# Kernel tuning notes

Hardware: AMD Instinct MI355X
Metric: run time of the kernel (lower is better)

The kernel has to match this reference:

```python
import jax, jax.numpy as jnp
import numpy as np

B, T, E, H, A, V = 32, 128, 256, 512, 256, 32000
S_SRC, S_CUE = 64, 64
OUT_IN = E + 2 * H + 2 * H  # emb + rnn_out + knowledge + src_ctx + cue_ctx (memory_size=H)
NEG = -1e9


def setup_inputs() -> dict:
    key = jax.random.key(0)
    ks = jax.random.split(key, 20)
    s = lambda k, sh: (jax.random.normal(k, sh) / np.sqrt(sh[0])).astype(jnp.float32)
    inp = {}
    inp['tokens'] = jax.random.randint(ks[0], (B, T), 0, V)
    inp['lengths'] = jax.random.randint(ks[1], (B,), 1, T + 1)
    inp['hidden0'] = jax.random.normal(ks[2], (B, H)) * 0.1
    inp['knowledge'] = jax.random.normal(ks[3], (B, H)) * 0.1
    inp['src_mem'] = jax.random.normal(ks[4], (B, S_SRC, H)) * 0.1
    inp['src_lengths'] = jax.random.randint(ks[5], (B,), 1, S_SRC + 1)
    inp['cue_mem'] = jax.random.normal(ks[6], (B, S_CUE, H)) * 0.1
    inp['cue_lengths'] = jax.random.randint(ks[7], (B,), 1, S_CUE + 1)
    # parameters
    inp['emb'] = jax.random.normal(ks[8], (V, E)) * 0.02
    inp['w_ih'] = s(ks[9], (E, 3 * H)); inp['w_hh'] = s(ks[10], (H, 3 * H))
    inp['b_ih'] = jnp.zeros((3 * H,)); inp['b_hh'] = jnp.zeros((3 * H,))
    Q = E + 2 * H
    inp['src_wq'] = s(ks[11], (Q, A)); inp['src_bq'] = jnp.zeros((A,))
    inp['src_wm'] = s(ks[12], (H, A)); inp['src_v'] = s(ks[13], (A,))
    inp['cue_wq'] = s(ks[14], (Q, A)); inp['cue_bq'] = jnp.zeros((A,))
    inp['cue_wm'] = s(ks[15], (H, A)); inp['cue_v'] = s(ks[16], (A,))
    inp['w_out1'] = s(ks[17], (OUT_IN, H)); inp['b_out1'] = jnp.zeros((H,))
    inp['w_out2'] = s(ks[18], (H, V)); inp['b_out2'] = jnp.zeros((V,))
    return inp


def _mlp_attn(q, mk, mem, wq, bq, v, mask):
    # q: (B,Q), mk = mem@wm precomputed: (B,S,A), mem: (B,S,H), mask: (B,S) True=valid
    scores = jnp.einsum('bsa,a->bs', jnp.tanh((q @ wq + bq)[:, None, :] + mk), v)
    scores = jnp.where(mask, scores, NEG)
    w = jax.nn.softmax(scores, axis=-1)
    return jnp.einsum('bs,bsh->bh', w, mem)


def reference(tokens, lengths, hidden0, knowledge, src_mem, src_lengths, cue_mem,
              cue_lengths, emb, w_ih, w_hh, b_ih, b_hh, src_wq, src_bq, src_wm,
              src_v, cue_wq, cue_bq, cue_wm, cue_v, w_out1, b_out1, w_out2, b_out2):
    x_all = emb[tokens]                                   # (B,T,E) teacher-forced embeddings
    valid = jnp.arange(T)[None, :] < lengths[:, None]     # (B,T)
    src_mask = jnp.arange(S_SRC)[None, :] < src_lengths[:, None]
    cue_mask = jnp.arange(S_CUE)[None, :] < cue_lengths[:, None]
    src_mk = src_mem @ src_wm                             # (B,S,A) hoisted memory projection
    cue_mk = cue_mem @ cue_wm

    def step(h, xs):
        x, vm = xs                                        # (B,E), (B,)
        gi = x @ w_ih + b_ih
        gh = h @ w_hh + b_hh
        i_r, i_z, i_n = jnp.split(gi, 3, axis=-1)
        h_r, h_z, h_n = jnp.split(gh, 3, axis=-1)
        r = jax.nn.sigmoid(i_r + h_r)
        z = jax.nn.sigmoid(i_z + h_z)
        n = jnp.tanh(i_n + r * h_n)
        h_new = (1.0 - z) * n + z * h                     # torch GRU cell
        q = jnp.concatenate([x, h, knowledge], axis=-1)   # query uses OLD hidden (as in source)
        src_ctx = _mlp_attn(q, src_mk, src_mem, src_wq, src_bq, src_v, src_mask)
        cue_ctx = _mlp_attn(q, cue_mk, cue_mem, cue_wq, cue_bq, cue_v, cue_mask)
        out_in = jnp.concatenate([x, h_new, knowledge, src_ctx, cue_ctx], axis=-1)
        vmc = vm[:, None]
        h_next = jnp.where(vmc, h_new, h)                 # only valid rows advance (length-sorted loop)
        return h_next, (jnp.where(vmc, out_in, 0.0), jnp.where(vmc, h_new, 0.0))

    h_final, (out_inputs, hid_mem) = jax.lax.scan(
        step, hidden0, (x_all.transpose(1, 0, 2), valid.T))
    out_inputs = out_inputs.transpose(1, 0, 2)            # (B,T,OUT_IN)
    hidden_memory = hid_mem.transpose(1, 0, 2)            # (B,T,H)
    logits = (out_inputs @ w_out1 + b_out1) @ w_out2 + b_out2
    log_probs = jax.nn.log_softmax(logits, axis=-1)       # (B,T,V)
    return log_probs, hidden_memory, h_final
```

## Files before the change

### kernel.cpp

```cpp
#include <hip/hip_runtime.h>

typedef unsigned int uint;
typedef unsigned short ushort;
using short8 = __attribute__((ext_vector_type(8))) short;
using f32x4  = __attribute__((ext_vector_type(4))) float;

#define DEVFN __device__ __forceinline__

constexpr int B_ = 32, T_ = 128, E_ = 256, H_ = 512, A_ = 256, V_ = 32000, S_ = 64;
constexpr int G3_ = 3 * H_;
constexpr int OUTIN_ = E_ + 4 * H_;
constexpr int M_ = B_ * T_;

DEVFN ushort f2b(float f) {
  uint u = __float_as_uint(f);
  u += 0x7fffu + ((u >> 16) & 1u);
  return (ushort)(u >> 16);
}
DEVFN float b2f(ushort b) { return __uint_as_float(((uint)b) << 16); }
DEVFN float sigmoid_f(float x) { return 1.f / (1.f + __expf(-x)); }
DEVFN float tanh_f(float x) { float e = __expf(2.f * x); return 1.f - 2.f / (e + 1.f); }

__global__ __launch_bounds__(256) void transpose_k(const float* __restrict__ in,
                                                   ushort* __restrict__ out, int R, int C) {
  __shared__ __align__(16) ushort tile[64][65];
  int c0 = blockIdx.x * 64, r0 = blockIdx.y * 64;
  int tx = threadIdx.x & 63, ty = threadIdx.x >> 6;
#pragma unroll
  for (int k = 0; k < 16; k++) {
    int i = ty + k * 4;
    int r = r0 + i, c = c0 + tx;
    if (r < R && c < C) tile[tx][i] = f2b(in[(size_t)r * C + c]);
  }
  __syncthreads();
#pragma unroll
  for (int k = 0; k < 16; k++) {
    int j = ty + k * 4;
    int c = c0 + j, r = r0 + tx;
    if (r < R && c < C) out[(size_t)c * R + r] = tile[j][tx];
  }
}

__global__ void convert_k(const float* __restrict__ in, ushort* __restrict__ out, int n) {
  int i = blockIdx.x * 256 + threadIdx.x;
  if (i < n) out[i] = f2b(in[i]);
}

__global__ __launch_bounds__(256) void gather_k(const int* __restrict__ tokens,
                                                const float* __restrict__ emb,
                                                ushort* __restrict__ xbf) {
  int r = blockIdx.x;
  int t = r >> 5, b = r & 31;
  int tok = tokens[b * T_ + t];
  xbf[(size_t)r * E_ + threadIdx.x] = f2b(emb[(size_t)tok * E_ + threadIdx.x]);
}

__global__ __launch_bounds__(256) void kq_k(const float* __restrict__ knowledge,
                                            const float* __restrict__ wq,
                                            const float* __restrict__ bq,
                                            float* __restrict__ kq) {
  int b = blockIdx.x, a = threadIdx.x;
  const float* kn = knowledge + b * H_;
  float s = 0.f;
  for (int h = 0; h < H_; h++) s += kn[h] * wq[(size_t)(E_ + H_ + h) * A_ + a];
  kq[b * A_ + a] = s + bq[a];
}

template <int OUTBF, int PERM, int HASBIAS>
__global__ __launch_bounds__(256) void gemm_bt(const ushort* __restrict__ Ag,
                                               const ushort* __restrict__ Btg,
                                               const float* __restrict__ bias,
                                               void* __restrict__ Cg, int M, int N, int K) {
  __shared__ __align__(16) ushort Ash[128][40];
  __shared__ __align__(16) ushort Bsh[128][40];
  const int nbx = gridDim.x;
  const int nwg = nbx * gridDim.y;
  const int lin = blockIdx.y * nbx + blockIdx.x;
  const int cpx = nwg >> 3;
  const int swz = (lin & 7) * cpx + (lin >> 3);
  const int m0 = (swz / nbx) * 128, n0 = (swz % nbx) * 128;
  const int tid = threadIdx.x;
  const int wave = tid >> 6, lane = tid & 63, lr = lane & 15, lg = lane >> 4;
  const int wr = wave >> 1, wc = wave & 1;
  f32x4 acc[4][4] = {};
  for (int kk = 0; kk < K; kk += 32) {
    {
      int r = tid >> 2, q = tid & 3;
      *(short8*)&Ash[r][q * 8] = *(const short8*)&Ag[(size_t)(m0 + r) * K + kk + q * 8];
      *(short8*)&Bsh[r][q * 8] = *(const short8*)&Btg[(size_t)(n0 + r) * K + kk + q * 8];
      r += 64;
      *(short8*)&Ash[r][q * 8] = *(const short8*)&Ag[(size_t)(m0 + r) * K + kk + q * 8];
      *(short8*)&Bsh[r][q * 8] = *(const short8*)&Btg[(size_t)(n0 + r) * K + kk + q * 8];
    }
    __syncthreads();
    short8 af[4], bfr[4];
#pragma unroll
    for (int mi = 0; mi < 4; mi++) af[mi] = *(const short8*)&Ash[wr * 64 + mi * 16 + lr][lg * 8];
#pragma unroll
    for (int ni = 0; ni < 4; ni++) bfr[ni] = *(const short8*)&Bsh[wc * 64 + ni * 16 + lr][lg * 8];
#pragma unroll
    for (int mi = 0; mi < 4; mi++)
#pragma unroll
      for (int ni = 0; ni < 4; ni++)
        acc[mi][ni] = __builtin_amdgcn_mfma_f32_16x16x32_bf16(af[mi], bfr[ni], acc[mi][ni], 0, 0, 0);
    __syncthreads();
  }
#pragma unroll
  for (int mi = 0; mi < 4; mi++)
#pragma unroll
    for (int ni = 0; ni < 4; ni++) {
      int col = n0 + wc * 64 + ni * 16 + lr;
      float bv = HASBIAS ? bias[col] : 0.f;
#pragma unroll
      for (int r = 0; r < 4; r++) {
        int row = m0 + wr * 64 + mi * 16 + lg * 4 + r;
        int orow = PERM ? ((row & 31) << 7) + (row >> 5) : row;
        float v = acc[mi][ni][r] + bv;
        if (OUTBF == 1)      ((ushort*)Cg)[(size_t)orow * N + col] = f2b(v);
        else if (OUTBF == 2) ((ushort*)Cg)[(size_t)orow * 2 * N + col] = f2b(v);
        else                 ((float*)Cg)[(size_t)orow * N + col] = v;
      }
    }
}

__global__ void inith_k(const float* __restrict__ h0, ushort* __restrict__ hpb) {
  int g = blockIdx.x * 256 + threadIdx.x;
  hpb[g] = f2b(h0[g]);
}

__global__ __launch_bounds__(128, 1) void scan_k(
    const float* __restrict__ w_hh, const float* __restrict__ b_hh,
    const float* __restrict__ gi, const int* __restrict__ lengths,
    const float* __restrict__ h0, ushort* hpb,
    float* __restrict__ hidmem, float* __restrict__ hfinal, uint* flags) {
  __shared__ __align__(16) ushort pk[2][16][16];
  const int wg = blockIdx.x;
  const int c0 = wg * 16;
  const int tid = threadIdx.x;
  const int wave = tid >> 6, lane = tid & 63, lr = lane & 15, lg = lane >> 4;
  const int c = c0 + lr;

  short8 wf0[16], wf1[16], wf2[16];
#pragma unroll
  for (int kk = 0; kk < 16; kk++) {
    short8 v0, v1, v2;
#pragma unroll
    for (int i = 0; i < 8; i++) {
      int k = kk * 32 + lg * 8 + i;
      v0[i] = (short)f2b(w_hh[(size_t)k * G3_ + 0 * H_ + c]);
      v1[i] = (short)f2b(w_hh[(size_t)k * G3_ + 1 * H_ + c]);
      v2[i] = (short)f2b(w_hh[(size_t)k * G3_ + 2 * H_ + c]);
    }
    wf0[kk] = v0; wf1[kk] = v1; wf2[kk] = v2;
  }
  const float bh0 = b_hh[c], bh1 = b_hh[H_ + c], bh2 = b_hh[2 * H_ + c];
  int len[4];
  float hp[4];
#pragma unroll
  for (int r = 0; r < 4; r++) {
    int bt = 16 * wave + lg * 4 + r;
    len[r] = lengths[bt];
    hp[r] = h0[(size_t)bt * H_ + c];
  }

  const uint fidx = ((uint)(lane & 31) * 2 + (uint)wave) * 32;

#pragma unroll 1
  for (int t = 0; t < T_; t++) {
    float g0[4], g1[4], g2[4];
#pragma unroll
    for (int r = 0; r < 4; r++) {
      int bt = 16 * wave + lg * 4 + r;
      const float* gr = gi + (size_t)(t * 32 + bt) * G3_ + c;
      g0[r] = gr[0]; g1[r] = gr[H_]; g2[r] = gr[2 * H_];
    }
    if (t > 0) {
      while (true) {
        uint f = __hip_atomic_load(&flags[fidx], __ATOMIC_RELAXED, __HIP_MEMORY_SCOPE_AGENT);
        if (__all((int)(f >= (uint)t))) break;
        __builtin_amdgcn_s_sleep(1);
      }
    }
    asm volatile("" ::: "memory");

    const ushort* Sb = hpb + (size_t)t * (B_ * H_);
    const int rowA = 16 * wave + lr;
    f32x4 a0 = {}, a1 = {}, a2 = {};
#pragma unroll
    for (int kk = 0; kk < 16; kk++) {
      short8 av = *(const short8*)(Sb + rowA * H_ + kk * 32 + lg * 8);
      a0 = __builtin_amdgcn_mfma_f32_16x16x32_bf16(av, wf0[kk], a0, 0, 0, 0);
      a1 = __builtin_amdgcn_mfma_f32_16x16x32_bf16(av, wf1[kk], a1, 0, 0, 0);
      a2 = __builtin_amdgcn_mfma_f32_16x16x32_bf16(av, wf2[kk], a2, 0, 0, 0);
    }

    ushort* Un16 = hpb + (size_t)(t + 1) * (B_ * H_);
    float hmv[4];
#pragma unroll
    for (int r = 0; r < 4; r++) {
      float rr = sigmoid_f(g0[r] + a0[r] + bh0);
      float zz = sigmoid_f(g1[r] + a1[r] + bh1);
      float nn = tanh_f(g2[r] + rr * (a2[r] + bh2));
      float hv = (1.f - zz) * nn + zz * hp[r];
      bool valid = t < len[r];
      float hx = valid ? hv : hp[r];
      hp[r] = hx;
      hmv[r] = valid ? hv : 0.f;
      pk[wave][lg * 4 + r][lr] = f2b(hx);
    }
    if (lane < 32) {
      int row = lane >> 1, half = lane & 1;
      short8 v = *(const short8*)&pk[wave][row][half * 8];
      ushort* gp = Un16 + ((size_t)(16 * wave + row) * H_ + c0 + half * 8);
      asm volatile("global_store_dwordx4 %0, %1, off sc1" :: "v"(gp), "v"(v) : "memory");
    }
    asm volatile("s_waitcnt vmcnt(0)" ::: "memory");
    if (lane == 0)
      __hip_atomic_store(&flags[(wg * 2 + wave) * 32], (uint)(t + 1),
                         __ATOMIC_RELAXED, __HIP_MEMORY_SCOPE_AGENT);
#pragma unroll
    for (int r = 0; r < 4; r++) {
      int bt = 16 * wave + lg * 4 + r;
      hidmem[((size_t)bt * T_ + t) * H_ + c] = hmv[r];
    }
  }
#pragma unroll
  for (int r = 0; r < 4; r++) {
    int bt = 16 * wave + lg * 4 + r;
    hfinal[(size_t)bt * H_ + c] = hp[r];
  }
}

__global__ __launch_bounds__(256) void attn_k(
    const float* __restrict__ qxk, const float* __restrict__ qh, const float* __restrict__ kq,
    const float* __restrict__ mk, const float* __restrict__ mem, const float* __restrict__ vvec,
    const int* __restrict__ slen, float* __restrict__ ctx) {
  __shared__ float qf[A_], vv[A_], sc[S_];
  int bx = blockIdx.x;
  int b = bx >> 7, t = bx & 127;
  int row = t * B_ + b;
  int tid = threadIdx.x;
  qf[tid] = qxk[(size_t)row * A_ + tid] + qh[(size_t)row * A_ + tid] + kq[b * A_ + tid];
  vv[tid] = vvec[tid];
  __syncthreads();
  int s = tid >> 2, q4 = tid & 3;
  const float* mkr = mk + ((size_t)(b * S_) + s) * A_;
  float part = 0.f;
#pragma unroll 4
  for (int i = 0; i < 64; i++) {
    int a = q4 + (i << 2);
    part += tanh_f(qf[a] + mkr[a]) * vv[a];
  }
  part += __shfl_xor(part, 1, 64);
  part += __shfl_xor(part, 2, 64);
  if (q4 == 0) sc[s] = part;
  __syncthreads();
  if (tid < S_) {
    float v = (tid < slen[b]) ? sc[tid] : -1e9f;
    float mm = v;
    for (int off = 1; off < 64; off <<= 1) mm = fmaxf(mm, __shfl_xor(mm, off, 64));
    float e = __expf(v - mm);
    float ss = e;
    for (int off = 1; off < 64; off <<= 1) ss += __shfl_xor(ss, off, 64);
    sc[tid] = e / ss;
  }
  __syncthreads();
  float c0 = 0.f, c1 = 0.f;
  const float* mb = mem + (size_t)b * S_ * H_;
  for (int ss2 = 0; ss2 < S_; ss2++) {
    float w = sc[ss2];
    c0 += w * mb[ss2 * H_ + tid];
    c1 += w * mb[ss2 * H_ + tid + 256];
  }
  ctx[(size_t)row * H_ + tid] = c0;
  ctx[(size_t)row * H_ + tid + 256] = c1;
}

__global__ __launch_bounds__(256) void assemble_k(
    const ushort* __restrict__ xbf, const float* __restrict__ hm,
    const float* __restrict__ knowledge, const float* __restrict__ ctxs,
    const float* __restrict__ ctxc, const int* __restrict__ lengths,
    ushort* __restrict__ outin) {
  int r = blockIdx.x;
  int t = r >> 5, b = r & 31;
  bool valid = t < lengths[b];
  int tid = threadIdx.x;
  ushort* dst = outin + (size_t)r * OUTIN_;
#pragma unroll
  for (int kblk = 0; kblk < 9; kblk++) {
    int i = kblk * 256 + tid;
    ushort v;
    if (i < E_)               v = xbf[(size_t)r * E_ + i];
    else if (i < E_ + H_)     v = f2b(hm[((size_t)b * T_ + t) * H_ + i - E_]);
    else if (i < E_ + 2 * H_) v = f2b(knowledge[b * H_ + i - (E_ + H_)]);
    else if (i < E_ + 3 * H_) v = f2b(ctxs[(size_t)r * H_ + i - (E_ + 2 * H_)]);
    else                      v = f2b(ctxc[(size_t)r * H_ + i - (E_ + 3 * H_)]);
    dst[i] = valid ? v : (ushort)0;
  }
}

__global__ __launch_bounds__(256) void logsoftmax_k(float* __restrict__ logits) {
  __shared__ float redm[4], reds[4];
  float* row = logits + (size_t)blockIdx.x * V_;
  const short8* rg = (const short8*)row;
  const int tid = threadIdx.x;
  short8 buf[16];
  float m = -3.4e38f, s = 0.f;
#pragma unroll
  for (int k = 0; k < 16; k++) {
    int i = tid + k * 256;
    if (i < V_ / 8) {
      short8 v = rg[i];
      buf[k] = v;
      float f0 = b2f((ushort)v[0]), f1 = b2f((ushort)v[1]);
      float f2 = b2f((ushort)v[2]), f3 = b2f((ushort)v[3]);
      float f4 = b2f((ushort)v[4]), f5 = b2f((ushort)v[5]);
      float f6 = b2f((ushort)v[6]), f7 = b2f((ushort)v[7]);
      float vm = fmaxf(fmaxf(fmaxf(f0, f1), fmaxf(f2, f3)),
                       fmaxf(fmaxf(f4, f5), fmaxf(f6, f7)));
      float nm = fmaxf(m, vm);
      s = s * __expf(m - nm) + __expf(f0 - nm) + __expf(f1 - nm) + __expf(f2 - nm) +
          __expf(f3 - nm) + __expf(f4 - nm) + __expf(f5 - nm) + __expf(f6 - nm) +
          __expf(f7 - nm);
      m = nm;
    }
  }
  for (int off = 1; off < 64; off <<= 1) {
    float om = __shfl_xor(m, off, 64), os = __shfl_xor(s, off, 64);
    float nm = fmaxf(m, om);
    s = s * __expf(m - nm) + os * __expf(om - nm);
    m = nm;
  }
  if ((tid & 63) == 0) { redm[tid >> 6] = m; reds[tid >> 6] = s; }
  __syncthreads();
  float M = fmaxf(fmaxf(redm[0], redm[1]), fmaxf(redm[2], redm[3]));
  float S = reds[0] * __expf(redm[0] - M) + reds[1] * __expf(redm[1] - M) +
            reds[2] * __expf(redm[2] - M) + reds[3] * __expf(redm[3] - M);
  float lse = M + __logf(S);
  __syncthreads();
#pragma unroll
  for (int k = 0; k < 16; k++) {
    int i = tid + k * 256;
    if (i < V_ / 8) {
      short8 v = buf[k];
      float4 o0, o1;
      o0.x = b2f((ushort)v[0]) - lse; o0.y = b2f((ushort)v[1]) - lse;
      o0.z = b2f((ushort)v[2]) - lse; o0.w = b2f((ushort)v[3]) - lse;
      o1.x = b2f((ushort)v[4]) - lse; o1.y = b2f((ushort)v[5]) - lse;
      o1.z = b2f((ushort)v[6]) - lse; o1.w = b2f((ushort)v[7]) - lse;
      *(float4*)&row[i * 8] = o0;
      *(float4*)&row[i * 8 + 4] = o1;
    }
  }
}

extern "C" void kernel_launch(void* const* d_in, const int* in_sizes, int n_in,
                              void* d_out, int out_size, void* d_ws, size_t ws_size,
                              hipStream_t stream) {
  const int*   tokens    = (const int*)  d_in[0];
  const int*   lengths   = (const int*)  d_in[1];
  const float* hidden0   = (const float*)d_in[2];
  const float* knowledge = (const float*)d_in[3];
  const float* src_mem   = (const float*)d_in[4];
  const int*   src_len   = (const int*)  d_in[5];
  const float* cue_mem   = (const float*)d_in[6];
  const int*   cue_len   = (const int*)  d_in[7];
  const float* emb       = (const float*)d_in[8];
  const float* w_ih      = (const float*)d_in[9];
  const float* w_hh      = (const float*)d_in[10];
  const float* b_ih      = (const float*)d_in[11];
  const float* b_hh      = (const float*)d_in[12];
  const float* src_wq    = (const float*)d_in[13];
  const float* src_bq    = (const float*)d_in[14];
  const float* src_wm    = (const float*)d_in[15];
  const float* src_v     = (const float*)d_in[16];
  const float* cue_wq    = (const float*)d_in[17];
  const float* cue_bq    = (const float*)d_in[18];
  const float* cue_wm    = (const float*)d_in[19];
  const float* cue_v     = (const float*)d_in[20];
  const float* w_out1    = (const float*)d_in[21];
  const float* b_out1    = (const float*)d_in[22];
  const float* w_out2    = (const float*)d_in[23];
  const float* b_out2    = (const float*)d_in[24];

  float* out_lp = (float*)d_out;
  float* out_hm = out_lp + (size_t)M_ * V_;
  float* out_hf = out_hm + (size_t)M_ * H_;

  char* scb = (char*)d_out;
  size_t off = 0;
  auto alloc = [&](size_t bytes) -> void* {
    void* p = scb + off;
    off = (off + bytes + 255) & ~(size_t)255;
    return p;
  };
  float*  GI    = (float*) alloc((size_t)M_ * G3_ * 4);
  float*  QXKs  = (float*) alloc((size_t)M_ * A_ * 4);
  float*  QXKc  = (float*) alloc((size_t)M_ * A_ * 4);
  float*  QHs   = (float*) alloc((size_t)M_ * A_ * 4);
  float*  QHc   = (float*) alloc((size_t)M_ * A_ * 4);
  float*  CTXs  = (float*) alloc((size_t)M_ * H_ * 4);
  float*  CTXc  = (float*) alloc((size_t)M_ * H_ * 4);
  ushort* OUTIN = (ushort*)alloc((size_t)M_ * OUTIN_ * 2);
  ushort* XBF   = (ushort*)alloc((size_t)M_ * E_ * 2);
  ushort* WIHT  = (ushort*)alloc((size_t)G3_ * E_ * 2);
  ushort* WQXTs = (ushort*)alloc((size_t)A_ * E_ * 2);
  ushort* WQXTc = (ushort*)alloc((size_t)A_ * E_ * 2);
  ushort* WQHTs = (ushort*)alloc((size_t)A_ * H_ * 2);
  ushort* WQHTc = (ushort*)alloc((size_t)A_ * H_ * 2);
  ushort* WMTs  = (ushort*)alloc((size_t)A_ * H_ * 2);
  ushort* WMTc  = (ushort*)alloc((size_t)A_ * H_ * 2);
  ushort* WO1T  = (ushort*)alloc((size_t)H_ * OUTIN_ * 2);
  ushort* MEMBs = (ushort*)alloc((size_t)B_ * S_ * H_ * 2);
  ushort* MEMBc = (ushort*)alloc((size_t)B_ * S_ * H_ * 2);
  float*  MKs   = (float*) alloc((size_t)B_ * S_ * A_ * 4);
  float*  MKc   = (float*) alloc((size_t)B_ * S_ * A_ * 4);
  float*  KQs   = (float*) alloc((size_t)B_ * A_ * 4);
  float*  KQc   = (float*) alloc((size_t)B_ * A_ * 4);
  ushort* HPB   = (ushort*)alloc((size_t)(T_ + 1) * B_ * H_ * 2);

  uint* FLAGS = (uint*)d_ws;
  ushort* WO2T = (ushort*)((char*)d_ws + 8192);
  ushort* HID1 = (ushort*)((char*)d_ws + 8192 + (size_t)V_ * H_ * 2);

  dim3 blk(256);
  hipMemsetAsync(FLAGS, 0, 8192, stream);

  transpose_k<<<dim3(G3_ / 64, E_ / 64), blk, 0, stream>>>(w_ih, WIHT, E_, G3_);
  transpose_k<<<dim3(A_ / 64, E_ / 64), blk, 0, stream>>>(src_wq, WQXTs, E_, A_);
  transpose_k<<<dim3(A_ / 64, H_ / 64), blk, 0, stream>>>(src_wq + (size_t)E_ * A_, WQHTs, H_, A_);
  transpose_k<<<dim3(A_ / 64, E_ / 64), blk, 0, stream>>>(cue_wq, WQXTc, E_, A_);
  transpose_k<<<dim3(A_ / 64, H_ / 64), blk, 0, stream>>>(cue_wq + (size_t)E_ * A_, WQHTc, H_, A_);
  transpose_k<<<dim3(A_ / 64, H_ / 64), blk, 0, stream>>>(src_wm, WMTs, H_, A_);
  transpose_k<<<dim3(A_ / 64, H_ / 64), blk, 0, stream>>>(cue_wm, WMTc, H_, A_);
  transpose_k<<<dim3(H_ / 64, OUTIN_ / 64), blk, 0, stream>>>(w_out1, WO1T, OUTIN_, H_);
  transpose_k<<<dim3(V_ / 64, H_ / 64), blk, 0, stream>>>(w_out2, WO2T, H_, V_);
  convert_k<<<(B_ * S_ * H_ + 255) / 256, blk, 0, stream>>>(src_mem, MEMBs, B_ * S_ * H_);
  convert_k<<<(B_ * S_ * H_ + 255) / 256, blk, 0, stream>>>(cue_mem, MEMBc, B_ * S_ * H_);

  gather_k<<<M_, blk, 0, stream>>>(tokens, emb, XBF);
  kq_k<<<B_, blk, 0, stream>>>(knowledge, src_wq, src_bq, KQs);
  kq_k<<<B_, blk, 0, stream>>>(knowledge, cue_wq, cue_bq, KQc);

  gemm_bt<0, 0, 1><<<dim3(G3_ / 128, M_ / 128), blk, 0, stream>>>(XBF, WIHT, b_ih, GI, M_, G3_, E_);
  gemm_bt<0, 0, 0><<<dim3(A_ / 128, M_ / 128), blk, 0, stream>>>(XBF, WQXTs, nullptr, QXKs, M_, A_, E_);
  gemm_bt<0, 0, 0><<<dim3(A_ / 128, M_ / 128), blk, 0, stream>>>(XBF, WQXTc, nullptr, QXKc, M_, A_, E_);
  gemm_bt<0, 0, 0><<<dim3(A_ / 128, (B_ * S_) / 128), blk, 0, stream>>>(MEMBs, WMTs, nullptr, MKs, B_ * S_, A_, H_);
  gemm_bt<0, 0, 0><<<dim3(A_ / 128, (B_ * S_) / 128), blk, 0, stream>>>(MEMBc, WMTc, nullptr, MKc, B_ * S_, A_, H_);

  inith_k<<<(B_ * H_) / 256, blk, 0, stream>>>(hidden0, HPB);
  scan_k<<<32, dim3(128), 0, stream>>>(w_hh, b_hh, GI, lengths, hidden0, HPB, out_hm, out_hf, FLAGS);

  gemm_bt<0, 0, 0><<<dim3(A_ / 128, M_ / 128), blk, 0, stream>>>(HPB, WQHTs, nullptr, QHs, M_, A_, H_);
  gemm_bt<0, 0, 0><<<dim3(A_ / 128, M_ / 128), blk, 0, stream>>>(HPB, WQHTc, nullptr, QHc, M_, A_, H_);
  attn_k<<<M_, blk, 0, stream>>>(QXKs, QHs, KQs, MKs, src_mem, src_v, src_len, CTXs);
  attn_k<<<M_, blk, 0, stream>>>(QXKc, QHc, KQc, MKc, cue_mem, cue_v, cue_len, CTXc);

  assemble_k<<<M_, blk, 0, stream>>>(XBF, out_hm, knowledge, CTXs, CTXc, lengths, OUTIN);
  gemm_bt<1, 0, 1><<<dim3(H_ / 128, M_ / 128), blk, 0, stream>>>(OUTIN, WO1T, b_out1, HID1, M_, H_, OUTIN_);
  gemm_bt<2, 1, 1><<<dim3(V_ / 128, M_ / 128), blk, 0, stream>>>(HID1, WO2T, b_out2, out_lp, M_, V_, H_);
  logsoftmax_k<<<M_, blk, 0, stream>>>(out_lp);
}
```

Baseline: 1.495 ms.

## Overlap independent prep work with the sequential GRU scan in one fused kernel

```diff
diff --git a/kernel.cpp b/kernel.cpp
--- a/kernel.cpp
+++ b/kernel.cpp
@@ -20,6 +20,9 @@
 DEVFN float b2f(ushort b) { return __uint_as_float(((uint)b) << 16); }
 DEVFN float sigmoid_f(float x) { return 1.f / (1.f + __expf(-x)); }
 DEVFN float tanh_f(float x) { float e = __expf(2.f * x); return 1.f - 2.f / (e + 1.f); }
+DEVFN f32x4 MFMA16(short8 a, short8 b, f32x4 c) {
+  return __builtin_amdgcn_mfma_f32_16x16x32_bf16(a, b, c, 0, 0, 0);
+}
 
 __global__ __launch_bounds__(256) void transpose_k(const float* __restrict__ in,
                                                    ushort* __restrict__ out, int R, int C) {
@@ -53,17 +56,6 @@
   int t = r >> 5, b = r & 31;
   int tok = tokens[b * T_ + t];
   xbf[(size_t)r * E_ + threadIdx.x] = f2b(emb[(size_t)tok * E_ + threadIdx.x]);
-}
-
-__global__ __launch_bounds__(256) void kq_k(const float* __restrict__ knowledge,
-                                            const float* __restrict__ wq,
-                                            const float* __restrict__ bq,
-                                            float* __restrict__ kq) {
-  int b = blockIdx.x, a = threadIdx.x;
-  const float* kn = knowledge + b * H_;
-  float s = 0.f;
-  for (int h = 0; h < H_; h++) s += kn[h] * wq[(size_t)(E_ + H_ + h) * A_ + a];
-  kq[b * A_ + a] = s + bq[a];
 }
 
 template <int OUTBF, int PERM, int HASBIAS>
@@ -102,7 +94,7 @@
     for (int mi = 0; mi < 4; mi++)
 #pragma unroll
       for (int ni = 0; ni < 4; ni++)
-        acc[mi][ni] = __builtin_amdgcn_mfma_f32_16x16x32_bf16(af[mi], bfr[ni], acc[mi][ni], 0, 0, 0);
+        acc[mi][ni] = MFMA16(af[mi], bfr[ni], acc[mi][ni]);
     __syncthreads();
   }
 #pragma unroll
@@ -128,15 +120,22 @@
   hpb[g] = f2b(h0[g]);
 }
 
-__global__ __launch_bounds__(128, 1) void scan_k(
-    const float* __restrict__ w_hh, const float* __restrict__ b_hh,
-    const float* __restrict__ gi, const int* __restrict__ lengths,
-    const float* __restrict__ h0, ushort* hpb,
-    float* __restrict__ hidmem, float* __restrict__ hfinal, uint* flags) {
-  __shared__ __align__(16) ushort pk[2][16][16];
-  const int wg = blockIdx.x;
+struct FArgs {
+  const float *w_hh, *b_hh, *gi, *h0;
+  const int* lengths;
+  ushort* hpb;
+  float *hidmem, *hfinal;
+  uint* flags;
+  const float *w_out1, *w_out2, *knowledge, *src_wq, *src_bq, *cue_wq, *cue_bq;
+  ushort *wo1t, *wo2t;
+  float *kqs, *kqc;
+  const ushort *xbf, *wqxts, *wqxtc, *membs, *membc, *wmts, *wmtc;
+  float *qxks, *qxkc, *mks, *mkc;
+};
+
+DEVFN void scan_body(const FArgs& P, int wg, int tid, char* smem) {
+  ushort (*pk)[16][16] = (ushort(*)[16][16])smem;
   const int c0 = wg * 16;
-  const int tid = threadIdx.x;
   const int wave = tid >> 6, lane = tid & 63, lr = lane & 15, lg = lane >> 4;
   const int c = c0 + lr;
 
@@ -147,22 +146,21 @@
 #pragma unroll
     for (int i = 0; i < 8; i++) {
       int k = kk * 32 + lg * 8 + i;
-      v0[i] = (short)f2b(w_hh[(size_t)k * G3_ + 0 * H_ + c]);
-      v1[i] = (short)f2b(w_hh[(size_t)k * G3_ + 1 * H_ + c]);
-      v2[i] = (short)f2b(w_hh[(size_t)k * G3_ + 2 * H_ + c]);
+      v0[i] = (short)f2b(P.w_hh[(size_t)k * G3_ + 0 * H_ + c]);
+      v1[i] = (short)f2b(P.w_hh[(size_t)k * G3_ + 1 * H_ + c]);
+      v2[i] = (short)f2b(P.w_hh[(size_t)k * G3_ + 2 * H_ + c]);
     }
     wf0[kk] = v0; wf1[kk] = v1; wf2[kk] = v2;
   }
-  const float bh0 = b_hh[c], bh1 = b_hh[H_ + c], bh2 = b_hh[2 * H_ + c];
+  const float bh0 = P.b_hh[c], bh1 = P.b_hh[H_ + c], bh2 = P.b_hh[2 * H_ + c];
   int len[4];
   float hp[4];
 #pragma unroll
   for (int r = 0; r < 4; r++) {
     int bt = 16 * wave + lg * 4 + r;
-    len[r] = lengths[bt];
-    hp[r] = h0[(size_t)bt * H_ + c];
-  }
-
+    len[r] = P.lengths[bt];
+    hp[r] = P.h0[(size_t)bt * H_ + c];
+  }
   const uint fidx = ((uint)(lane & 31) * 2 + (uint)wave) * 32;
 
 #pragma unroll 1
@@ -171,30 +169,30 @@
 #pragma unroll
     for (int r = 0; r < 4; r++) {
       int bt = 16 * wave + lg * 4 + r;
-      const float* gr = gi + (size_t)(t * 32 + bt) * G3_ + c;
+      const float* gr = P.gi + (size_t)(t * 32 + bt) * G3_ + c;
       g0[r] = gr[0]; g1[r] = gr[H_]; g2[r] = gr[2 * H_];
     }
     if (t > 0) {
       while (true) {
-        uint f = __hip_atomic_load(&flags[fidx], __ATOMIC_RELAXED, __HIP_MEMORY_SCOPE_AGENT);
+        uint f = __hip_atomic_load(&P.flags[fidx], __ATOMIC_RELAXED, __HIP_MEMORY_SCOPE_AGENT);
         if (__all((int)(f >= (uint)t))) break;
         __builtin_amdgcn_s_sleep(1);
       }
     }
     asm volatile("" ::: "memory");
 
-    const ushort* Sb = hpb + (size_t)t * (B_ * H_);
+    const ushort* Sb = P.hpb + (size_t)t * (B_ * H_);
     const int rowA = 16 * wave + lr;
     f32x4 a0 = {}, a1 = {}, a2 = {};
 #pragma unroll
     for (int kk = 0; kk < 16; kk++) {
       short8 av = *(const short8*)(Sb + rowA * H_ + kk * 32 + lg * 8);
-      a0 = __builtin_amdgcn_mfma_f32_16x16x32_bf16(av, wf0[kk], a0, 0, 0, 0);
-      a1 = __builtin_amdgcn_mfma_f32_16x16x32_bf16(av, wf1[kk], a1, 0, 0, 0);
-      a2 = __builtin_amdgcn_mfma_f32_16x16x32_bf16(av, wf2[kk], a2, 0, 0, 0);
-    }
-
-    ushort* Un16 = hpb + (size_t)(t + 1) * (B_ * H_);
+      a0 = MFMA16(av, wf0[kk], a0);
+      a1 = MFMA16(av, wf1[kk], a1);
+      a2 = MFMA16(av, wf2[kk], a2);
+    }
+
+    ushort* Un16 = P.hpb + (size_t)(t + 1) * (B_ * H_);
     float hmv[4];
 #pragma unroll
     for (int r = 0; r < 4; r++) {
@@ -216,24 +214,128 @@
     }
     asm volatile("s_waitcnt vmcnt(0)" ::: "memory");
     if (lane == 0)
-      __hip_atomic_store(&flags[(wg * 2 + wave) * 32], (uint)(t + 1),
+      __hip_atomic_store(&P.flags[(wg * 2 + wave) * 32], (uint)(t + 1),
                          __ATOMIC_RELAXED, __HIP_MEMORY_SCOPE_AGENT);
 #pragma unroll
     for (int r = 0; r < 4; r++) {
       int bt = 16 * wave + lg * 4 + r;
-      hidmem[((size_t)bt * T_ + t) * H_ + c] = hmv[r];
+      P.hidmem[((size_t)bt * T_ + t) * H_ + c] = hmv[r];
     }
   }
 #pragma unroll
   for (int r = 0; r < 4; r++) {
     int bt = 16 * wave + lg * 4 + r;
-    hfinal[(size_t)bt * H_ + c] = hp[r];
+    P.hfinal[(size_t)bt * H_ + c] = hp[r];
+  }
+}
+
+DEVFN void trans_tile(const float* in, ushort* out, int R, int C, int bx, int by,
+                      int tid, char* smem) {
+  ushort (*tile)[65] = (ushort(*)[65])smem;
+  int c0 = bx * 64, r0 = by * 64;
+  int tx = tid & 63, ty = tid >> 6;
+#pragma unroll
+  for (int k = 0; k < 16; k++) {
+    int i = ty + k * 4;
+    int r = r0 + i, c = c0 + tx;
+    if (r < R && c < C) tile[tx][i] = f2b(in[(size_t)r * C + c]);
+  }
+  __syncthreads();
+#pragma unroll
+  for (int k = 0; k < 16; k++) {
+    int j = ty + k * 4;
+    int c = c0 + j, r = r0 + tx;
+    if (r < R && c < C) out[(size_t)c * R + r] = tile[j][tx];
+  }
+  __syncthreads();
+}
+
+DEVFN void kq_job(const float* knowledge, const float* wq, const float* bq,
+                  float* kq, int b, int tid) {
+  const float* kn = knowledge + b * H_;
+  float s = 0.f;
+  for (int h = 0; h < H_; h++) s += kn[h] * wq[(size_t)(E_ + H_ + h) * A_ + tid];
+  kq[b * A_ + tid] = s + bq[tid];
+}
+
+DEVFN void gemm_tile(const ushort* Ag, const ushort* Btg, float* Cg,
+                     int N, int K, int m0, int n0, int tid, char* smem) {
+  ushort (*Ash)[40] = (ushort(*)[40])smem;
+  ushort (*Bsh)[40] = (ushort(*)[40])(smem + 10240);
+  const int wave = tid >> 6, lane = tid & 63, lr = lane & 15, lg = lane >> 4;
+  const int wr = wave >> 1, wc = wave & 1;
+  f32x4 acc[4][4] = {};
+  for (int kk = 0; kk < K; kk += 32) {
+    {
+      int r = tid >> 2, q = tid & 3;
+      *(short8*)&Ash[r][q * 8] = *(const short8*)&Ag[(size_t)(m0 + r) * K + kk + q * 8];
+      *(short8*)&Bsh[r][q * 8] = *(const short8*)&Btg[(size_t)(n0 + r) * K + kk + q * 8];
+      r += 64;
+      *(short8*)&Ash[r][q * 8] = *(const short8*)&Ag[(size_t)(m0 + r) * K + kk + q * 8];
+      *(short8*)&Bsh[r][q * 8] = *(const short8*)&Btg[(size_t)(n0 + r) * K + kk + q * 8];
+    }
+    __syncthreads();
+    short8 af[4], bfr[4];
+#pragma unroll
+    for (int mi = 0; mi < 4; mi++) af[mi] = *(const short8*)&Ash[wr * 64 + mi * 16 + lr][lg * 8];
+#pragma unroll
+    for (int ni = 0; ni < 4; ni++) bfr[ni] = *(const short8*)&Bsh[wc * 64 + ni * 16 + lr][lg * 8];
+#pragma unroll
+    for (int mi = 0; mi < 4; mi++)
+#pragma unroll
+      for (int ni = 0; ni < 4; ni++)
+        acc[mi][ni] = MFMA16(af[mi], bfr[ni], acc[mi][ni]);
+    __syncthreads();
+  }
+#pragma unroll
+  for (int mi = 0; mi < 4; mi++)
+#pragma unroll
+    for (int ni = 0; ni < 4; ni++) {
+      int col = n0 + wc * 64 + ni * 16 + lr;
+#pragma unroll
+      for (int r = 0; r < 4; r++) {
+        int row = m0 + wr * 64 + mi * 16 + lg * 4 + r;
+        Cg[(size_t)row * N + col] = acc[mi][ni][r];
+      }
+    }
+}
+
+constexpr int NJOB = 288 + 4000 + 64 + 128 + 64;
+
+__global__ __launch_bounds__(256, 1) void scanfused_k(FArgs P) {
+  __shared__ __align__(16) char smem[20480];
+  const int bid = blockIdx.x, tid = threadIdx.x;
+  if (bid < 32) {
+    if (tid < 128) scan_body(P, bid, tid, smem);
+    return;
+  }
+  for (int j = bid - 32; j < NJOB; j += 224) {
+    if (j < 288) {
+      trans_tile(P.w_out1, P.wo1t, OUTIN_, H_, j & 7, j >> 3, tid, smem);
+    } else if (j < 4288) {
+      int q = j - 288;
+      trans_tile(P.w_out2, P.wo2t, H_, V_, q % 500, q / 500, tid, smem);
+    } else if (j < 4352) {
+      int q = j - 4288;
+      if (q < 32) kq_job(P.knowledge, P.src_wq, P.src_bq, P.kqs, q, tid);
+      else        kq_job(P.knowledge, P.cue_wq, P.cue_bq, P.kqc, q - 32, tid);
+    } else if (j < 4480) {
+      int q = j - 4352;
+      int mat = q >> 6; q &= 63;
+      gemm_tile(P.xbf, mat ? P.wqxtc : P.wqxts, mat ? P.qxkc : P.qxks,
+                A_, E_, (q >> 1) * 128, (q & 1) * 128, tid, smem);
+    } else {
+      int q = j - 4480;
+      int mat = q >> 5; q &= 31;
+      gemm_tile(mat ? P.membc : P.membs, mat ? P.wmtc : P.wmts, mat ? P.mkc : P.mks,
+                A_, H_, (q >> 1) * 128, (q & 1) * 128, tid, smem);
+    }
   }
 }
 
 __global__ __launch_bounds__(256) void attn_k(
     const float* __restrict__ qxk, const float* __restrict__ qh, const float* __restrict__ kq,
-    const float* __restrict__ mk, const float* __restrict__ mem, const float* __restrict__ vvec,
+    const float* __restrict__ mk, const ushort* __restrict__ memb, const float* __restrict__ vvec,
     const int* __restrict__ slen, float* __restrict__ ctx) {
   __shared__ float qf[A_], vv[A_], sc[S_];
   int bx = blockIdx.x;
@@ -266,11 +368,11 @@
   }
   __syncthreads();
   float c0 = 0.f, c1 = 0.f;
-  const float* mb = mem + (size_t)b * S_ * H_;
+  const ushort* mb = memb + (size_t)b * S_ * H_;
   for (int ss2 = 0; ss2 < S_; ss2++) {
     float w = sc[ss2];
-    c0 += w * mb[ss2 * H_ + tid];
-    c1 += w * mb[ss2 * H_ + tid + 256];
+    c0 += w * b2f(mb[ss2 * H_ + tid]);
+    c1 += w * b2f(mb[ss2 * H_ + tid + 256]);
   }
   ctx[(size_t)row * H_ + tid] = c0;
   ctx[(size_t)row * H_ + tid + 256] = c1;
@@ -433,28 +535,28 @@
   transpose_k<<<dim3(A_ / 64, H_ / 64), blk, 0, stream>>>(cue_wq + (size_t)E_ * A_, WQHTc, H_, A_);
   transpose_k<<<dim3(A_ / 64, H_ / 64), blk, 0, stream>>>(src_wm, WMTs, H_, A_);
   transpose_k<<<dim3(A_ / 64, H_ / 64), blk, 0, stream>>>(cue_wm, WMTc, H_, A_);
-  transpose_k<<<dim3(H_ / 64, OUTIN_ / 64), blk, 0, stream>>>(w_out1, WO1T, OUTIN_, H_);
-  transpose_k<<<dim3(V_ / 64, H_ / 64), blk, 0, stream>>>(w_out2, WO2T, H_, V_);
   convert_k<<<(B_ * S_ * H_ + 255) / 256, blk, 0, stream>>>(src_mem, MEMBs, B_ * S_ * H_);
   convert_k<<<(B_ * S_ * H_ + 255) / 256, blk, 0, stream>>>(cue_mem, MEMBc, B_ * S_ * H_);
-
   gather_k<<<M_, blk, 0, stream>>>(tokens, emb, XBF);
-  kq_k<<<B_, blk, 0, stream>>>(knowledge, src_wq, src_bq, KQs);
-  kq_k<<<B_, blk, 0, stream>>>(knowledge, cue_wq, cue_bq, KQc);
 
   gemm_bt<0, 0, 1><<<dim3(G3_ / 128, M_ / 128), blk, 0, stream>>>(XBF, WIHT, b_ih, GI, M_, G3_, E_);
-  gemm_bt<0, 0, 0><<<dim3(A_ / 128, M_ / 128), blk, 0, stream>>>(XBF, WQXTs, nullptr, QXKs, M_, A_, E_);
-  gemm_bt<0, 0, 0><<<dim3(A_ / 128, M_ / 128), blk, 0, stream>>>(XBF, WQXTc, nullptr, QXKc, M_, A_, E_);
-  gemm_bt<0, 0, 0><<<dim3(A_ / 128, (B_ * S_) / 128), blk, 0, stream>>>(MEMBs, WMTs, nullptr, MKs, B_ * S_, A_, H_);
-  gemm_bt<0, 0, 0><<<dim3(A_ / 128, (B_ * S_) / 128), blk, 0, stream>>>(MEMBc, WMTc, nullptr, MKc, B_ * S_, A_, H_);
-
   inith_k<<<(B_ * H_) / 256, blk, 0, stream>>>(hidden0, HPB);
-  scan_k<<<32, dim3(128), 0, stream>>>(w_hh, b_hh, GI, lengths, hidden0, HPB, out_hm, out_hf, FLAGS);
+
+  FArgs P;
+  P.w_hh = w_hh; P.b_hh = b_hh; P.gi = GI; P.h0 = hidden0;
+  P.lengths = lengths; P.hpb = HPB; P.hidmem = out_hm; P.hfinal = out_hf; P.flags = FLAGS;
+  P.w_out1 = w_out1; P.w_out2 = w_out2; P.knowledge = knowledge;
+  P.src_wq = src_wq; P.src_bq = src_bq; P.cue_wq = cue_wq; P.cue_bq = cue_bq;
+  P.wo1t = WO1T; P.wo2t = WO2T; P.kqs = KQs; P.kqc = KQc;
+  P.xbf = XBF; P.wqxts = WQXTs; P.wqxtc = WQXTc;
+  P.membs = MEMBs; P.membc = MEMBc; P.wmts = WMTs; P.wmtc = WMTc;
+  P.qxks = QXKs; P.qxkc = QXKc; P.mks = MKs; P.mkc = MKc;
+  scanfused_k<<<dim3(256), blk, 0, stream>>>(P);
 
   gemm_bt<0, 0, 0><<<dim3(A_ / 128, M_ / 128), blk, 0, stream>>>(HPB, WQHTs, nullptr, QHs, M_, A_, H_);
   gemm_bt<0, 0, 0><<<dim3(A_ / 128, M_ / 128), blk, 0, stream>>>(HPB, WQHTc, nullptr, QHc, M_, A_, H_);
-  attn_k<<<M_, blk, 0, stream>>>(QXKs, QHs, KQs, MKs, src_mem, src_v, src_len, CTXs);
-  attn_k<<<M_, blk, 0, stream>>>(QXKc, QHc, KQc, MKc, cue_mem, cue_v, cue_len, CTXc);
+  attn_k<<<M_, blk, 0, stream>>>(QXKs, QHs, KQs, MKs, MEMBs, src_v, src_len, CTXs);
+  attn_k<<<M_, blk, 0, stream>>>(QXKc, QHc, KQc, MKc, MEMBc, cue_v, cue_len, CTXc);
 
   assemble_k<<<M_, blk, 0, stream>>>(XBF, out_hm, knowledge, CTXs, CTXc, lengths, OUTIN);
   gemm_bt<1, 0, 1><<<dim3(H_ / 128, M_ / 128), blk, 0, stream>>>(OUTIN, WO1T, b_out1, HID1, M_, H_, OUTIN_);
```

Result: faster. 1.400 ms (-6.3%).
